# Kernel tuning notes

Hardware: AMD Instinct MI355X
Metric: run time of the kernel (lower is better)

The kernel has to match this reference:

```python
import jax, jax.numpy as jnp
import numpy as np

N_NODES = 100000


def setup_inputs() -> dict:
    key = jax.random.key(0)
    k_x, k_r, k_c, k_v, k_t = jax.random.split(key, 5)
    n_edges = 3200000
    fin, fout = 512, 128
    x = jax.random.normal(k_x, (N_NODES, fin), dtype=jnp.float32)
    rows = jax.random.randint(k_r, (n_edges,), 0, N_NODES, dtype=jnp.int32)
    cols = jax.random.randint(k_c, (n_edges,), 0, N_NODES, dtype=jnp.int32)
    vals = jax.random.uniform(k_v, (n_edges,), dtype=jnp.float32)
    theta = jax.random.normal(k_t, (fin, fout), dtype=jnp.float32) * (1.0 / np.sqrt(fin))
    bias = jnp.zeros((fout,), dtype=jnp.float32)
    return {"x": x, "rows": rows, "cols": cols, "vals": vals, "theta": theta, "bias": bias}


def reference(x, rows, cols, vals, theta, bias):
    # SpMM: mx[i] = sum over edges (i <- j) of A[i,j] * x[j]
    gathered = vals[:, None] * x[cols]                      # [E, fin]
    mx = jax.ops.segment_sum(gathered, rows, num_segments=N_NODES)  # [N, fin]
    # Dense feature transform + bias + relu
    o = jnp.einsum('nf,fo->no', mx, theta) + bias           # [N, fout]
    return jax.nn.relu(o)
```

## Files before the change

### kernel.cpp

```cpp
#include <hip/hip_runtime.h>
#include <stdint.h>
#include <stddef.h>

#define FIN 512
#define FOUT 128
#define BROWS 160
#define SORT_CAP 7680
#define TILE 4096
#define SCHUNK 1024

typedef __attribute__((ext_vector_type(8))) short short8;
typedef __attribute__((ext_vector_type(4))) float f32x4;

__device__ __forceinline__ unsigned short f2bf(float f) {
  unsigned u = __builtin_bit_cast(unsigned, f);
  u = (u + 0x7fffu + ((u >> 16) & 1u)) >> 16;
  return (unsigned short)u;
}
__device__ __forceinline__ float bf2f(unsigned short h) {
  unsigned u = ((unsigned)h) << 16;
  return __builtin_bit_cast(float, u);
}

__global__ void prep_theta_k(const float* __restrict__ theta,
                             unsigned short* __restrict__ thetaT) {
  int idx = blockIdx.x * blockDim.x + threadIdx.x;
  int n = idx >> 9;
  int k = idx & 511;
  thetaT[idx] = f2bf(theta[k * FOUT + n]);
}

__global__ __launch_bounds__(256) void gemm_k(const float* __restrict__ x,
                                              const unsigned short* __restrict__ thetaT,
                                              unsigned short* __restrict__ yb, int M) {
  __shared__ __align__(16) unsigned short lA[128 * 40];
  __shared__ __align__(16) unsigned short lB[128 * 40];
  const int tid = threadIdx.x;
  const int row0 = blockIdx.x * 128;
  const int wave = tid >> 6, lane = tid & 63;
  const int wm = wave >> 1, wn = wave & 1;
  const int fr = lane & 15, fq = lane >> 4;
  const int arow = tid >> 1, ahalf = tid & 1;

  f32x4 acc[4][4] = {};

  const int grow = row0 + arow;
  const bool aval = (grow < M);
  const float* asrc = x + (size_t)(aval ? grow : 0) * FIN + ahalf * 16;
  const unsigned short* bsrc = thetaT + (size_t)arow * FIN + ahalf * 16;

  for (int k0 = 0; k0 < FIN; k0 += 32) {
    float av[16];
    if (aval) {
      const float4* p = (const float4*)(asrc + k0);
      float4 v0 = p[0], v1 = p[1], v2 = p[2], v3 = p[3];
      av[0] = v0.x; av[1] = v0.y; av[2] = v0.z; av[3] = v0.w;
      av[4] = v1.x; av[5] = v1.y; av[6] = v1.z; av[7] = v1.w;
      av[8] = v2.x; av[9] = v2.y; av[10] = v2.z; av[11] = v2.w;
      av[12] = v3.x; av[13] = v3.y; av[14] = v3.z; av[15] = v3.w;
    } else {
      for (int i = 0; i < 16; i++) av[i] = 0.f;
    }
    unsigned ap[8];
    for (int i = 0; i < 8; i++)
      ap[i] = (unsigned)f2bf(av[2 * i]) | ((unsigned)f2bf(av[2 * i + 1]) << 16);
    uint4* aw = (uint4*)&lA[arow * 40 + ahalf * 16];
    aw[0] = make_uint4(ap[0], ap[1], ap[2], ap[3]);
    aw[1] = make_uint4(ap[4], ap[5], ap[6], ap[7]);

    const uint4* bp = (const uint4*)(bsrc + k0);
    uint4 b0 = bp[0], b1 = bp[1];
    uint4* bw = (uint4*)&lB[arow * 40 + ahalf * 16];
    bw[0] = b0; bw[1] = b1;

    __syncthreads();

    short8 af[4], bfv[4];
#pragma unroll
    for (int m = 0; m < 4; m++)
      af[m] = *(const short8*)&lA[(wm * 64 + m * 16 + fr) * 40 + fq * 8];
#pragma unroll
    for (int n = 0; n < 4; n++)
      bfv[n] = *(const short8*)&lB[(wn * 64 + n * 16 + fr) * 40 + fq * 8];
#pragma unroll
    for (int m = 0; m < 4; m++)
#pragma unroll
      for (int n = 0; n < 4; n++)
        acc[m][n] = __builtin_amdgcn_mfma_f32_16x16x32_bf16(af[m], bfv[n], acc[m][n], 0, 0, 0);

    __syncthreads();
  }

#pragma unroll
  for (int m = 0; m < 4; m++) {
    int rbase = row0 + wm * 64 + m * 16 + fq * 4;
#pragma unroll
    for (int j = 0; j < 4; j++) {
      int r = rbase + j;
      if (r < M) {
        unsigned short* dst = yb + (size_t)r * FOUT + wn * 64;
#pragma unroll
        for (int n = 0; n < 4; n++) dst[n * 16 + fr] = f2bf(acc[m][n][j]);
      }
    }
  }
}

__global__ __launch_bounds__(256) void chist_k(const int* __restrict__ rows,
                                               int* __restrict__ cnt,
                                               int E, int NT, int NB) {
  __shared__ int lh[1024];
  int c = blockIdx.x, t = threadIdx.x;
  for (int i = t; i < NB; i += 256) lh[i] = 0;
  __syncthreads();
  int base = c * TILE;
#pragma unroll
  for (int k = 0; k < TILE / 256; k++) {
    int i = base + k * 256 + t;
    if (i < E) atomicAdd(&lh[rows[i] / BROWS], 1);
  }
  __syncthreads();
  for (int j = t; j < NB; j += 256) cnt[(size_t)j * NT + c] = lh[j];
}

__global__ __launch_bounds__(256) void scan_partial_k(const int* __restrict__ counts,
                                                      int* __restrict__ blockSums, int N) {
  int base = blockIdx.x * SCHUNK;
  int t = threadIdx.x;
  int s = 0;
#pragma unroll
  for (int i = 0; i < SCHUNK / 256; i++) {
    int idx = base + t + i * 256;
    s += (idx < N) ? counts[idx] : 0;
  }
  for (int off = 32; off; off >>= 1) s += __shfl_down(s, off, 64);
  __shared__ int ws[4];
  if ((t & 63) == 0) ws[t >> 6] = s;
  __syncthreads();
  if (t == 0) blockSums[blockIdx.x] = ws[0] + ws[1] + ws[2] + ws[3];
}

__global__ __launch_bounds__(1024) void scan_sums_k(int* __restrict__ blockSums, int nb) {
  __shared__ int tmp[1024];
  int t = threadIdx.x;
  tmp[t] = (t < nb) ? blockSums[t] : 0;
  __syncthreads();
  for (int off = 1; off < 1024; off <<= 1) {
    int v = (t >= off) ? tmp[t - off] : 0;
    __syncthreads();
    tmp[t] += v;
    __syncthreads();
  }
  if (t < nb) blockSums[t] = (t == 0) ? 0 : tmp[t - 1];
}

__global__ __launch_bounds__(256) void scan_final_k(const int* __restrict__ counts,
                                                    const int* __restrict__ blockSums,
                                                    int* __restrict__ pos, int N) {
  int b = blockIdx.x;
  int t = threadIdx.x;
  int idx = b * SCHUNK + t * 4;
  int v0 = (idx + 0 < N) ? counts[idx + 0] : 0;
  int v1 = (idx + 1 < N) ? counts[idx + 1] : 0;
  int v2 = (idx + 2 < N) ? counts[idx + 2] : 0;
  int v3 = (idx + 3 < N) ? counts[idx + 3] : 0;
  int local = v0 + v1 + v2 + v3;

  int lane = t & 63, w = t >> 6;
  int inc = local;
  for (int off = 1; off < 64; off <<= 1) {
    int u = __shfl_up(inc, off, 64);
    if (lane >= off) inc += u;
  }
  __shared__ int wsum[4];
  if (lane == 63) wsum[w] = inc;
  __syncthreads();
  int woff = 0;
  for (int i = 0; i < 4; i++)
    if (i < w) woff += wsum[i];
  int run = blockSums[b] + woff + inc - local;

  if (idx + 0 < N) pos[idx + 0] = run; run += v0;
  if (idx + 1 < N) pos[idx + 1] = run; run += v1;
  if (idx + 2 < N) pos[idx + 2] = run; run += v2;
  if (idx + 3 < N) pos[idx + 3] = run; run += v3;
}

__global__ __launch_bounds__(256) void bmeta_k(const int* __restrict__ pos,
                                               int* __restrict__ boff,
                                               int* __restrict__ offsets,
                                               int NB, int NT, int E, int M) {
  int t = threadIdx.x;
  for (int b = t; b < NB; b += 256) boff[b] = pos[(size_t)b * NT];
  if (t == 0) {
    boff[NB] = E;
    offsets[M] = E;
  }
}

__global__ __launch_bounds__(256) void cscatter_k(const int* __restrict__ rows,
                                                  const int* __restrict__ cols,
                                                  const float* __restrict__ vals,
                                                  const int* __restrict__ pos,
                                                  unsigned* __restrict__ rec4,
                                                  unsigned char* __restrict__ rlo,
                                                  int E, int NT, int NB) {
  __shared__ int cur[1024];
  int c = blockIdx.x, t = threadIdx.x;
  for (int i = t; i < NB; i += 256) cur[i] = pos[(size_t)i * NT + c];
  __syncthreads();
  int base = c * TILE;
#pragma unroll
  for (int k = 0; k < TILE / 256; k++) {
    int i = base + k * 256 + t;
    if (i < E) {
      int r = rows[i];
      int b = r / BROWS;
      int p = atomicAdd(&cur[b], 1);
      rec4[p] = ((unsigned)cols[i] << 15) | ((unsigned)f2bf(vals[i]) & 0x7fffu);
      rlo[p] = (unsigned char)(r - b * BROWS);
    }
  }
}

__global__ __launch_bounds__(256) void bsort_k(const int* __restrict__ boff,
                                               unsigned* __restrict__ rec4,
                                               const unsigned char* __restrict__ rlo,
                                               int* __restrict__ offsets, int M) {
  __shared__ unsigned s4[SORT_CAP];
  __shared__ unsigned char k8[SORT_CAP];
  __shared__ int lh[256];
  __shared__ int lsc[256];
  int b = blockIdx.x, t = threadIdx.x;
  int start = boff[b], end = boff[b + 1];
  int n = end - start;
  if (n > SORT_CAP) n = SORT_CAP;

  for (int i = t; i < n; i += 256) {
    s4[i] = rec4[start + i];
    k8[i] = rlo[start + i];
  }
  lh[t] = 0;
  __syncthreads();
  for (int i = t; i < n; i += 256) atomicAdd(&lh[k8[i]], 1);
  __syncthreads();
  lsc[t] = lh[t];
  __syncthreads();
  for (int off = 1; off < 256; off <<= 1) {
    int v = (t >= off) ? lsc[t - off] : 0;
    __syncthreads();
    lsc[t] += v;
    __syncthreads();
  }
  int excl = t ? lsc[t - 1] : 0;
  int row = b * BROWS + t;
  if (t < BROWS && row < M) offsets[row] = start + excl;
  lh[t] = excl;
  __syncthreads();
  for (int i = t; i < n; i += 256) {
    unsigned r = s4[i];
    int p = atomicAdd(&lh[k8[i]], 1);
    rec4[start + p] = r;
  }
}

__global__ __launch_bounds__(256) void rowv2_k(const int* __restrict__ offsets,
                                               const unsigned* __restrict__ rec4,
                                               const unsigned short* __restrict__ yb,
                                               const float* __restrict__ bias,
                                               float* __restrict__ out, int M) {
  int gid = blockIdx.x * blockDim.x + threadIdx.x;
  int r = gid >> 4;
  int l = gid & 15;
  if (r >= M) return;
  int s = offsets[r], e = offsets[r + 1];
  const unsigned short* src = yb + l * 8;

  float a0 = 0.f, a1 = 0.f, a2 = 0.f, a3 = 0.f, a4 = 0.f, a5 = 0.f, a6 = 0.f, a7 = 0.f;
  float c0 = 0.f, c1 = 0.f, c2 = 0.f, c3 = 0.f, c4 = 0.f, c5 = 0.f, c6 = 0.f, c7 = 0.f;

  int i = s;
  for (; i + 2 <= e; i += 2) {
    unsigned q0 = rec4[i];
    unsigned q1 = rec4[i + 1];
    const uint4 u0 = *(const uint4*)(src + (size_t)(q0 >> 15) * FOUT);
    const uint4 u1 = *(const uint4*)(src + (size_t)(q1 >> 15) * FOUT);
    float v0 = __builtin_bit_cast(float, (q0 & 0x7fffu) << 16);
    float v1 = __builtin_bit_cast(float, (q1 & 0x7fffu) << 16);
    a0 += v0 * __builtin_bit_cast(float, u0.x << 16);
    a1 += v0 * __builtin_bit_cast(float, u0.x & 0xffff0000u);
    a2 += v0 * __builtin_bit_cast(float, u0.y << 16);
    a3 += v0 * __builtin_bit_cast(float, u0.y & 0xffff0000u);
    a4 += v0 * __builtin_bit_cast(float, u0.z << 16);
    a5 += v0 * __builtin_bit_cast(float, u0.z & 0xffff0000u);
    a6 += v0 * __builtin_bit_cast(float, u0.w << 16);
    a7 += v0 * __builtin_bit_cast(float, u0.w & 0xffff0000u);
    c0 += v1 * __builtin_bit_cast(float, u1.x << 16);
    c1 += v1 * __builtin_bit_cast(float, u1.x & 0xffff0000u);
    c2 += v1 * __builtin_bit_cast(float, u1.y << 16);
    c3 += v1 * __builtin_bit_cast(float, u1.y & 0xffff0000u);
    c4 += v1 * __builtin_bit_cast(float, u1.z << 16);
    c5 += v1 * __builtin_bit_cast(float, u1.z & 0xffff0000u);
    c6 += v1 * __builtin_bit_cast(float, u1.w << 16);
    c7 += v1 * __builtin_bit_cast(float, u1.w & 0xffff0000u);
  }
  if (i < e) {
    unsigned q0 = rec4[i];
    const uint4 u0 = *(const uint4*)(src + (size_t)(q0 >> 15) * FOUT);
    float v0 = __builtin_bit_cast(float, (q0 & 0x7fffu) << 16);
    a0 += v0 * __builtin_bit_cast(float, u0.x << 16);
    a1 += v0 * __builtin_bit_cast(float, u0.x & 0xffff0000u);
    a2 += v0 * __builtin_bit_cast(float, u0.y << 16);
    a3 += v0 * __builtin_bit_cast(float, u0.y & 0xffff0000u);
    a4 += v0 * __builtin_bit_cast(float, u0.z << 16);
    a5 += v0 * __builtin_bit_cast(float, u0.z & 0xffff0000u);
    a6 += v0 * __builtin_bit_cast(float, u0.w << 16);
    a7 += v0 * __builtin_bit_cast(float, u0.w & 0xffff0000u);
  }

  const float4 b0 = *(const float4*)(bias + l * 8);
  const float4 b1 = *(const float4*)(bias + l * 8 + 4);
  float* dst = out + (size_t)r * FOUT + l * 8;
  float4 o0, o1;
  o0.x = fmaxf(a0 + c0 + b0.x, 0.f);
  o0.y = fmaxf(a1 + c1 + b0.y, 0.f);
  o0.z = fmaxf(a2 + c2 + b0.z, 0.f);
  o0.w = fmaxf(a3 + c3 + b0.w, 0.f);
  o1.x = fmaxf(a4 + c4 + b1.x, 0.f);
  o1.y = fmaxf(a5 + c5 + b1.y, 0.f);
  o1.z = fmaxf(a6 + c6 + b1.z, 0.f);
  o1.w = fmaxf(a7 + c7 + b1.w, 0.f);
  *(float4*)(dst) = o0;
  *(float4*)(dst + 4) = o1;
}

extern "C" void kernel_launch(void* const* d_in, const int* in_sizes, int n_in,
                              void* d_out, int out_size, void* d_ws, size_t ws_size,
                              hipStream_t stream) {
  const float* x = (const float*)d_in[0];
  const int* rows = (const int*)d_in[1];
  const int* cols = (const int*)d_in[2];
  const float* vals = (const float*)d_in[3];
  const float* theta = (const float*)d_in[4];
  const float* bias = (const float*)d_in[5];
  float* out = (float*)d_out;
  const int M = in_sizes[0] / FIN;
  const int E = in_sizes[1];
  const int NB = (M + BROWS - 1) / BROWS;
  const int NT = (E + TILE - 1) / TILE;

  char* w = (char*)d_ws;
  auto alloc = [&](size_t bytes) {
    char* p = w;
    w += (bytes + 255) & ~(size_t)255;
    return p;
  };
  unsigned short* yb = (unsigned short*)alloc((size_t)M * FOUT * 2);
  unsigned short* thetaT = (unsigned short*)alloc((size_t)FIN * FOUT * 2);
  int* cnt = (int*)alloc((size_t)NB * NT * 4);
  int* pos = (int*)alloc((size_t)NB * NT * 4);
  int* boff = (int*)alloc((size_t)(NB + 1) * 4);
  int* offsets = (int*)alloc((size_t)(M + 1) * 4);
  unsigned* rec4 = (unsigned*)alloc((size_t)E * 4);
  unsigned char* rlo = (unsigned char*)alloc((size_t)E);
  const int NSCAN = NB * NT;
  const int nb2 = (NSCAN + SCHUNK - 1) / SCHUNK;
  int* blockSums = (int*)alloc((size_t)nb2 * 4);

  prep_theta_k<<<(FIN * FOUT) / 256, 256, 0, stream>>>(theta, thetaT);
  gemm_k<<<(M + 127) / 128, 256, 0, stream>>>(x, thetaT, yb, M);
  chist_k<<<NT, 256, 0, stream>>>(rows, cnt, E, NT, NB);
  scan_partial_k<<<nb2, 256, 0, stream>>>(cnt, blockSums, NSCAN);
  scan_sums_k<<<1, 1024, 0, stream>>>(blockSums, nb2);
  scan_final_k<<<nb2, 256, 0, stream>>>(cnt, blockSums, pos, NSCAN);
  bmeta_k<<<1, 256, 0, stream>>>(pos, boff, offsets, NB, NT, E, M);
  cscatter_k<<<NT, 256, 0, stream>>>(rows, cols, vals, pos, rec4, rlo, E, NT, NB);
  bsort_k<<<NB, 256, 0, stream>>>(boff, rec4, rlo, offsets, M);
  rowv2_k<<<(M * 16 + 255) / 256, 256, 0, stream>>>(offsets, rec4, yb, bias, out, M);
}
```

Baseline: 361.9 us.

## Coarsen bucket-count matrix to edge slices and scatter via global atomic cursors

Replaces the per-tile bucket count matrix (NB x NT) with a coarser NB x K matrix where K counts 128K-edge slices. Tile histograms are merged into it with global atomics, and the scatter claims slots through global atomic cursors instead of per-block shared-memory cursors. The aim is to shrink the prefix scan and the count/pos traffic. The cost is a memset, contended global atomics in the scatter, and a scatter order within a bucket that is no longer deterministic (bsort sorts it afterwards).

Result: slower. 412.3 us (+13.9%).

```diff
diff --git a/kernel.cpp b/kernel.cpp
--- a/kernel.cpp
+++ b/kernel.cpp
@@ -7,6 +7,7 @@
 #define BROWS 160
 #define SORT_CAP 7680
 #define TILE 4096
+#define SLICE_SHIFT 17
 #define SCHUNK 1024
 
 typedef __attribute__((ext_vector_type(8))) short short8;
@@ -107,20 +108,22 @@
 }
 
 __global__ __launch_bounds__(256) void chist_k(const int* __restrict__ rows,
-                                               int* __restrict__ cnt,
-                                               int E, int NT, int NB) {
+                                               int* __restrict__ cnt2,
+                                               int E, int K) {
   __shared__ int lh[1024];
   int c = blockIdx.x, t = threadIdx.x;
-  for (int i = t; i < NB; i += 256) lh[i] = 0;
+  int k = c >> 5;
+  for (int i = t; i < 1024; i += 256) lh[i] = 0;
   __syncthreads();
   int base = c * TILE;
 #pragma unroll
-  for (int k = 0; k < TILE / 256; k++) {
-    int i = base + k * 256 + t;
+  for (int kk = 0; kk < TILE / 256; kk++) {
+    int i = base + kk * 256 + t;
     if (i < E) atomicAdd(&lh[rows[i] / BROWS], 1);
   }
   __syncthreads();
-  for (int j = t; j < NB; j += 256) cnt[(size_t)j * NT + c] = lh[j];
+  for (int j = t; j < 1024; j += 256)
+    if (lh[j]) atomicAdd(&cnt2[(size_t)j * K + k], lh[j]);
 }
 
 __global__ __launch_bounds__(256) void scan_partial_k(const int* __restrict__ counts,
@@ -156,7 +159,8 @@
 
 __global__ __launch_bounds__(256) void scan_final_k(const int* __restrict__ counts,
                                                     const int* __restrict__ blockSums,
-                                                    int* __restrict__ pos, int N) {
+                                                    int* __restrict__ pos,
+                                                    int* __restrict__ gcur, int N) {
   int b = blockIdx.x;
   int t = threadIdx.x;
   int idx = b * SCHUNK + t * 4;
@@ -180,18 +184,18 @@
     if (i < w) woff += wsum[i];
   int run = blockSums[b] + woff + inc - local;
 
-  if (idx + 0 < N) pos[idx + 0] = run; run += v0;
-  if (idx + 1 < N) pos[idx + 1] = run; run += v1;
-  if (idx + 2 < N) pos[idx + 2] = run; run += v2;
-  if (idx + 3 < N) pos[idx + 3] = run; run += v3;
+  if (idx + 0 < N) { pos[idx + 0] = run; gcur[idx + 0] = run; } run += v0;
+  if (idx + 1 < N) { pos[idx + 1] = run; gcur[idx + 1] = run; } run += v1;
+  if (idx + 2 < N) { pos[idx + 2] = run; gcur[idx + 2] = run; } run += v2;
+  if (idx + 3 < N) { pos[idx + 3] = run; gcur[idx + 3] = run; } run += v3;
 }
 
 __global__ __launch_bounds__(256) void bmeta_k(const int* __restrict__ pos,
                                                int* __restrict__ boff,
                                                int* __restrict__ offsets,
-                                               int NB, int NT, int E, int M) {
+                                               int NB, int K, int E, int M) {
   int t = threadIdx.x;
-  for (int b = t; b < NB; b += 256) boff[b] = pos[(size_t)b * NT];
+  for (int b = t; b < NB; b += 256) boff[b] = pos[(size_t)b * K];
   if (t == 0) {
     boff[NB] = E;
     offsets[M] = E;
@@ -201,25 +205,19 @@
 __global__ __launch_bounds__(256) void cscatter_k(const int* __restrict__ rows,
                                                   const int* __restrict__ cols,
                                                   const float* __restrict__ vals,
-                                                  const int* __restrict__ pos,
+                                                  int* __restrict__ gcur,
                                                   unsigned* __restrict__ rec4,
                                                   unsigned char* __restrict__ rlo,
-                                                  int E, int NT, int NB) {
-  __shared__ int cur[1024];
-  int c = blockIdx.x, t = threadIdx.x;
-  for (int i = t; i < NB; i += 256) cur[i] = pos[(size_t)i * NT + c];
-  __syncthreads();
-  int base = c * TILE;
-#pragma unroll
-  for (int k = 0; k < TILE / 256; k++) {
-    int i = base + k * 256 + t;
-    if (i < E) {
-      int r = rows[i];
-      int b = r / BROWS;
-      int p = atomicAdd(&cur[b], 1);
-      rec4[p] = ((unsigned)cols[i] << 15) | ((unsigned)f2bf(vals[i]) & 0x7fffu);
-      rlo[p] = (unsigned char)(r - b * BROWS);
-    }
+                                                  int E, int K) {
+  int i = blockIdx.x * blockDim.x + threadIdx.x;
+  int st = gridDim.x * blockDim.x;
+  for (; i < E; i += st) {
+    int r = rows[i];
+    int b = r / BROWS;
+    int k = i >> SLICE_SHIFT;
+    int p = atomicAdd(&gcur[(size_t)b * K + k], 1);
+    rec4[p] = ((unsigned)cols[i] << 15) | ((unsigned)f2bf(vals[i]) & 0x7fffu);
+    rlo[p] = (unsigned char)(r - b * BROWS);
   }
 }
 
@@ -348,6 +346,7 @@
   const int E = in_sizes[1];
   const int NB = (M + BROWS - 1) / BROWS;
   const int NT = (E + TILE - 1) / TILE;
+  const int K = (E + (1 << SLICE_SHIFT) - 1) >> SLICE_SHIFT;
 
   char* w = (char*)d_ws;
   auto alloc = [&](size_t bytes) {
@@ -357,24 +356,26 @@
   };
   unsigned short* yb = (unsigned short*)alloc((size_t)M * FOUT * 2);
   unsigned short* thetaT = (unsigned short*)alloc((size_t)FIN * FOUT * 2);
-  int* cnt = (int*)alloc((size_t)NB * NT * 4);
-  int* pos = (int*)alloc((size_t)NB * NT * 4);
+  const int NSCAN = NB * K;
+  int* cnt2 = (int*)alloc((size_t)NSCAN * 4);
+  int* pos = (int*)alloc((size_t)NSCAN * 4);
+  int* gcur = (int*)alloc((size_t)NSCAN * 4);
   int* boff = (int*)alloc((size_t)(NB + 1) * 4);
   int* offsets = (int*)alloc((size_t)(M + 1) * 4);
   unsigned* rec4 = (unsigned*)alloc((size_t)E * 4);
   unsigned char* rlo = (unsigned char*)alloc((size_t)E);
-  const int NSCAN = NB * NT;
   const int nb2 = (NSCAN + SCHUNK - 1) / SCHUNK;
   int* blockSums = (int*)alloc((size_t)nb2 * 4);
 
+  hipMemsetAsync(cnt2, 0, (size_t)NSCAN * 4, stream);
   prep_theta_k<<<(FIN * FOUT) / 256, 256, 0, stream>>>(theta, thetaT);
   gemm_k<<<(M + 127) / 128, 256, 0, stream>>>(x, thetaT, yb, M);
-  chist_k<<<NT, 256, 0, stream>>>(rows, cnt, E, NT, NB);
-  scan_partial_k<<<nb2, 256, 0, stream>>>(cnt, blockSums, NSCAN);
+  chist_k<<<NT, 256, 0, stream>>>(rows, cnt2, E, K);
+  scan_partial_k<<<nb2, 256, 0, stream>>>(cnt2, blockSums, NSCAN);
   scan_sums_k<<<1, 1024, 0, stream>>>(blockSums, nb2);
-  scan_final_k<<<nb2, 256, 0, stream>>>(cnt, blockSums, pos, NSCAN);
-  bmeta_k<<<1, 256, 0, stream>>>(pos, boff, offsets, NB, NT, E, M);
-  cscatter_k<<<NT, 256, 0, stream>>>(rows, cols, vals, pos, rec4, rlo, E, NT, NB);
+  scan_final_k<<<nb2, 256, 0, stream>>>(cnt2, blockSums, pos, gcur, NSCAN);
+  bmeta_k<<<1, 256, 0, stream>>>(pos, boff, offsets, NB, K, E, M);
+  cscatter_k<<<2048, 256, 0, stream>>>(rows, cols, vals, gcur, rec4, rlo, E, K);
   bsort_k<<<NB, 256, 0, stream>>>(boff, rec4, rlo, offsets, M);
   rowv2_k<<<(M * 16 + 255) / 256, 256, 0, stream>>>(offsets, rec4, yb, bias, out, M);
 }
```

## Replace global bucket scan and scatter with per-tile LDS bucket sort plus merge

Applied to the files above, without the earlier changes.

Edges are now bucketed in a single tile-local pass. Each 8192-edge tile histograms, scans and scatters its records into shared memory, then writes them contiguously along with per-tile bucket offsets. One small kernel sums the per-bucket totals. The bucket-sort kernel then gathers each bucket's segments from all tiles before doing the row-level sort. This drops the multi-kernel global scan (histogram, three scan passes, meta, scatter) and the random global scatter. In exchange, bucket-sort threads run serial per-tile copy loops, the single-block totals kernel loops over all ~391 tiles, and NBK is hardcoded to 625 buckets.

After: 344.2 us. -4.9%, faster.

```diff
diff --git a/kernel.cpp b/kernel.cpp
--- a/kernel.cpp
+++ b/kernel.cpp
@@ -5,9 +5,9 @@
 #define FIN 512
 #define FOUT 128
 #define BROWS 160
+#define NBK 625
 #define SORT_CAP 7680
-#define TILE 4096
-#define SCHUNK 1024
+#define TILE 8192
 
 typedef __attribute__((ext_vector_type(8))) short short8;
 typedef __attribute__((ext_vector_type(4))) float f32x4;
@@ -106,142 +106,170 @@
   }
 }
 
-__global__ __launch_bounds__(256) void chist_k(const int* __restrict__ rows,
-                                               int* __restrict__ cnt,
-                                               int E, int NT, int NB) {
-  __shared__ int lh[1024];
-  int c = blockIdx.x, t = threadIdx.x;
-  for (int i = t; i < NB; i += 256) lh[i] = 0;
-  __syncthreads();
-  int base = c * TILE;
+__global__ __launch_bounds__(256) void tilesort_k(const int* __restrict__ rows,
+                                                  const int* __restrict__ cols,
+                                                  const float* __restrict__ vals,
+                                                  unsigned* __restrict__ rec4tile,
+                                                  unsigned char* __restrict__ rlotile,
+                                                  int* __restrict__ lofs, int E) {
+  __shared__ int hist[NBK];
+  __shared__ int wsum[4];
+  __shared__ unsigned srec[TILE];
+  __shared__ unsigned char srlo[TILE];
+  const int c = blockIdx.x, t = threadIdx.x;
+  const int base = c * TILE;
+  const int n = (E - base < TILE) ? (E - base) : TILE;
+
+  for (int i = t; i < NBK; i += 256) hist[i] = 0;
+  __syncthreads();
+
 #pragma unroll
   for (int k = 0; k < TILE / 256; k++) {
     int i = base + k * 256 + t;
-    if (i < E) atomicAdd(&lh[rows[i] / BROWS], 1);
-  }
-  __syncthreads();
-  for (int j = t; j < NB; j += 256) cnt[(size_t)j * NT + c] = lh[j];
-}
-
-__global__ __launch_bounds__(256) void scan_partial_k(const int* __restrict__ counts,
-                                                      int* __restrict__ blockSums, int N) {
-  int base = blockIdx.x * SCHUNK;
-  int t = threadIdx.x;
-  int s = 0;
-#pragma unroll
-  for (int i = 0; i < SCHUNK / 256; i++) {
-    int idx = base + t + i * 256;
-    s += (idx < N) ? counts[idx] : 0;
-  }
-  for (int off = 32; off; off >>= 1) s += __shfl_down(s, off, 64);
-  __shared__ int ws[4];
-  if ((t & 63) == 0) ws[t >> 6] = s;
-  __syncthreads();
-  if (t == 0) blockSums[blockIdx.x] = ws[0] + ws[1] + ws[2] + ws[3];
-}
-
-__global__ __launch_bounds__(1024) void scan_sums_k(int* __restrict__ blockSums, int nb) {
-  __shared__ int tmp[1024];
-  int t = threadIdx.x;
-  tmp[t] = (t < nb) ? blockSums[t] : 0;
-  __syncthreads();
-  for (int off = 1; off < 1024; off <<= 1) {
-    int v = (t >= off) ? tmp[t - off] : 0;
-    __syncthreads();
-    tmp[t] += v;
-    __syncthreads();
-  }
-  if (t < nb) blockSums[t] = (t == 0) ? 0 : tmp[t - 1];
-}
-
-__global__ __launch_bounds__(256) void scan_final_k(const int* __restrict__ counts,
-                                                    const int* __restrict__ blockSums,
-                                                    int* __restrict__ pos, int N) {
-  int b = blockIdx.x;
-  int t = threadIdx.x;
-  int idx = b * SCHUNK + t * 4;
-  int v0 = (idx + 0 < N) ? counts[idx + 0] : 0;
-  int v1 = (idx + 1 < N) ? counts[idx + 1] : 0;
-  int v2 = (idx + 2 < N) ? counts[idx + 2] : 0;
-  int v3 = (idx + 3 < N) ? counts[idx + 3] : 0;
-  int local = v0 + v1 + v2 + v3;
-
-  int lane = t & 63, w = t >> 6;
-  int inc = local;
+    if (i < E) atomicAdd(&hist[rows[i] / BROWS], 1);
+  }
+  __syncthreads();
+
+  int c0 = t * 3, c1 = c0 + 1, c2 = c0 + 2;
+  int h0 = (c0 < NBK) ? hist[c0] : 0;
+  int h1 = (c1 < NBK) ? hist[c1] : 0;
+  int h2 = (c2 < NBK) ? hist[c2] : 0;
+  int loc = h0 + h1 + h2;
+  int lane = t & 63, wv = t >> 6;
+  int inc = loc;
   for (int off = 1; off < 64; off <<= 1) {
     int u = __shfl_up(inc, off, 64);
     if (lane >= off) inc += u;
   }
-  __shared__ int wsum[4];
-  if (lane == 63) wsum[w] = inc;
-  __syncthreads();
-  int woff = 0;
+  if (lane == 63) wsum[wv] = inc;
+  __syncthreads();
+  int excl = inc - loc;
   for (int i = 0; i < 4; i++)
-    if (i < w) woff += wsum[i];
-  int run = blockSums[b] + woff + inc - local;
-
-  if (idx + 0 < N) pos[idx + 0] = run; run += v0;
-  if (idx + 1 < N) pos[idx + 1] = run; run += v1;
-  if (idx + 2 < N) pos[idx + 2] = run; run += v2;
-  if (idx + 3 < N) pos[idx + 3] = run; run += v3;
-}
-
-__global__ __launch_bounds__(256) void bmeta_k(const int* __restrict__ pos,
-                                               int* __restrict__ boff,
-                                               int* __restrict__ offsets,
-                                               int NB, int NT, int E, int M) {
-  int t = threadIdx.x;
-  for (int b = t; b < NB; b += 256) boff[b] = pos[(size_t)b * NT];
-  if (t == 0) {
-    boff[NB] = E;
-    offsets[M] = E;
-  }
-}
-
-__global__ __launch_bounds__(256) void cscatter_k(const int* __restrict__ rows,
-                                                  const int* __restrict__ cols,
-                                                  const float* __restrict__ vals,
-                                                  const int* __restrict__ pos,
-                                                  unsigned* __restrict__ rec4,
-                                                  unsigned char* __restrict__ rlo,
-                                                  int E, int NT, int NB) {
-  __shared__ int cur[1024];
-  int c = blockIdx.x, t = threadIdx.x;
-  for (int i = t; i < NB; i += 256) cur[i] = pos[(size_t)i * NT + c];
-  __syncthreads();
-  int base = c * TILE;
+    if (i < wv) excl += wsum[i];
+
+  size_t lbase = (size_t)c * (NBK + 1);
+  int e = excl;
+  if (c0 <= NBK) lofs[lbase + c0] = e;
+  __syncthreads();
+  if (c0 < NBK) hist[c0] = e;
+  e += h0;
+  if (c1 <= NBK) lofs[lbase + c1] = e;
+  if (c1 < NBK) hist[c1] = e;
+  e += h1;
+  if (c2 <= NBK) lofs[lbase + c2] = e;
+  if (c2 < NBK) hist[c2] = e;
+  __syncthreads();
+
 #pragma unroll
   for (int k = 0; k < TILE / 256; k++) {
     int i = base + k * 256 + t;
     if (i < E) {
       int r = rows[i];
       int b = r / BROWS;
-      int p = atomicAdd(&cur[b], 1);
-      rec4[p] = ((unsigned)cols[i] << 15) | ((unsigned)f2bf(vals[i]) & 0x7fffu);
-      rlo[p] = (unsigned char)(r - b * BROWS);
-    }
+      int p = atomicAdd(&hist[b], 1);
+      srec[p] = ((unsigned)cols[i] << 15) | ((unsigned)f2bf(vals[i]) & 0x7fffu);
+      srlo[p] = (unsigned char)(r - b * BROWS);
+    }
+  }
+  __syncthreads();
+
+  for (int j = t; j < n; j += 256) {
+    rec4tile[base + j] = srec[j];
+    rlotile[base + j] = srlo[j];
+  }
+}
+
+__global__ __launch_bounds__(1024) void btot_k(const int* __restrict__ lofs,
+                                               int* __restrict__ boff,
+                                               int* __restrict__ offsets,
+                                               int NT, int E, int M) {
+  __shared__ int tmp[1024];
+  int t = threadIdx.x;
+  int s = 0;
+  if (t < NBK) {
+    for (int c = 0; c < NT; c++) {
+      size_t lb = (size_t)c * (NBK + 1) + t;
+      s += lofs[lb + 1] - lofs[lb];
+    }
+  }
+  tmp[t] = s;
+  __syncthreads();
+  for (int off = 1; off < 1024; off <<= 1) {
+    int v = (t >= off) ? tmp[t - off] : 0;
+    __syncthreads();
+    tmp[t] += v;
+    __syncthreads();
+  }
+  if (t < NBK) boff[t] = (t == 0) ? 0 : tmp[t - 1];
+  if (t == 0) {
+    boff[NBK] = E;
+    offsets[M] = E;
   }
 }
 
 __global__ __launch_bounds__(256) void bsort_k(const int* __restrict__ boff,
-                                               unsigned* __restrict__ rec4,
-                                               const unsigned char* __restrict__ rlo,
-                                               int* __restrict__ offsets, int M) {
+                                               const int* __restrict__ lofs,
+                                               const unsigned* __restrict__ rec4tile,
+                                               const unsigned char* __restrict__ rlotile,
+                                               unsigned* __restrict__ rec4s,
+                                               int* __restrict__ offsets,
+                                               int NT, int M) {
   __shared__ unsigned s4[SORT_CAP];
   __shared__ unsigned char k8[SORT_CAP];
   __shared__ int lh[256];
   __shared__ int lsc[256];
+  __shared__ int wsum[4];
   int b = blockIdx.x, t = threadIdx.x;
-  int start = boff[b], end = boff[b + 1];
-  int n = end - start;
+  int start = boff[b];
+
+  int ca = 2 * t, cb = 2 * t + 1;
+  int la = 0, fa = 0, lb2 = 0, fb = 0;
+  if (ca < NT) {
+    size_t p = (size_t)ca * (NBK + 1) + b;
+    la = lofs[p];
+    fa = lofs[p + 1] - la;
+  }
+  if (cb < NT) {
+    size_t p = (size_t)cb * (NBK + 1) + b;
+    lb2 = lofs[p];
+    fb = lofs[p + 1] - lb2;
+  }
+  int loc = fa + fb;
+  int lane = t & 63, wv = t >> 6;
+  int inc = loc;
+  for (int off = 1; off < 64; off <<= 1) {
+    int u = __shfl_up(inc, off, 64);
+    if (lane >= off) inc += u;
+  }
+  if (lane == 63) wsum[wv] = inc;
+  __syncthreads();
+  int excl = inc - loc;
+  for (int i = 0; i < 4; i++)
+    if (i < wv) excl += wsum[i];
+
+  if (ca < NT) {
+    const unsigned* src = rec4tile + (size_t)ca * TILE + la;
+    const unsigned char* srl = rlotile + (size_t)ca * TILE + la;
+    for (int j = 0; j < fa; j++) {
+      int d = excl + j;
+      if (d < SORT_CAP) { s4[d] = src[j]; k8[d] = srl[j]; }
+    }
+    excl += fa;
+  }
+  if (cb < NT) {
+    const unsigned* src = rec4tile + (size_t)cb * TILE + lb2;
+    const unsigned char* srl = rlotile + (size_t)cb * TILE + lb2;
+    for (int j = 0; j < fb; j++) {
+      int d = excl + j;
+      if (d < SORT_CAP) { s4[d] = src[j]; k8[d] = srl[j]; }
+    }
+  }
+
+  int n = boff[b + 1] - start;
   if (n > SORT_CAP) n = SORT_CAP;
-
-  for (int i = t; i < n; i += 256) {
-    s4[i] = rec4[start + i];
-    k8[i] = rlo[start + i];
-  }
   lh[t] = 0;
   __syncthreads();
+
   for (int i = t; i < n; i += 256) atomicAdd(&lh[k8[i]], 1);
   __syncthreads();
   lsc[t] = lh[t];
@@ -252,15 +280,15 @@
     lsc[t] += v;
     __syncthreads();
   }
-  int excl = t ? lsc[t - 1] : 0;
+  int ex = t ? lsc[t - 1] : 0;
   int row = b * BROWS + t;
-  if (t < BROWS && row < M) offsets[row] = start + excl;
-  lh[t] = excl;
+  if (t < BROWS && row < M) offsets[row] = start + ex;
+  lh[t] = ex;
   __syncthreads();
   for (int i = t; i < n; i += 256) {
     unsigned r = s4[i];
     int p = atomicAdd(&lh[k8[i]], 1);
-    rec4[start + p] = r;
+    rec4s[start + p] = r;
   }
 }
 
@@ -346,7 +374,6 @@
   float* out = (float*)d_out;
   const int M = in_sizes[0] / FIN;
   const int E = in_sizes[1];
-  const int NB = (M + BROWS - 1) / BROWS;
   const int NT = (E + TILE - 1) / TILE;
 
   char* w = (char*)d_ws;
@@ -357,24 +384,17 @@
   };
   unsigned short* yb = (unsigned short*)alloc((size_t)M * FOUT * 2);
   unsigned short* thetaT = (unsigned short*)alloc((size_t)FIN * FOUT * 2);
-  int* cnt = (int*)alloc((size_t)NB * NT * 4);
-  int* pos = (int*)alloc((size_t)NB * NT * 4);
-  int* boff = (int*)alloc((size_t)(NB + 1) * 4);
+  unsigned* rec4tile = (unsigned*)alloc((size_t)NT * TILE * 4);
+  unsigned char* rlotile = (unsigned char*)alloc((size_t)NT * TILE);
+  int* lofs = (int*)alloc((size_t)NT * (NBK + 1) * 4);
+  int* boff = (int*)alloc((size_t)(NBK + 1) * 4);
   int* offsets = (int*)alloc((size_t)(M + 1) * 4);
-  unsigned* rec4 = (unsigned*)alloc((size_t)E * 4);
-  unsigned char* rlo = (unsigned char*)alloc((size_t)E);
-  const int NSCAN = NB * NT;
-  const int nb2 = (NSCAN + SCHUNK - 1) / SCHUNK;
-  int* blockSums = (int*)alloc((size_t)nb2 * 4);
+  unsigned* rec4s = (unsigned*)alloc((size_t)E * 4);
 
   prep_theta_k<<<(FIN * FOUT) / 256, 256, 0, stream>>>(theta, thetaT);
   gemm_k<<<(M + 127) / 128, 256, 0, stream>>>(x, thetaT, yb, M);
-  chist_k<<<NT, 256, 0, stream>>>(rows, cnt, E, NT, NB);
-  scan_partial_k<<<nb2, 256, 0, stream>>>(cnt, blockSums, NSCAN);
-  scan_sums_k<<<1, 1024, 0, stream>>>(blockSums, nb2);
-  scan_final_k<<<nb2, 256, 0, stream>>>(cnt, blockSums, pos, NSCAN);
-  bmeta_k<<<1, 256, 0, stream>>>(pos, boff, offsets, NB, NT, E, M);
-  cscatter_k<<<NT, 256, 0, stream>>>(rows, cols, vals, pos, rec4, rlo, E, NT, NB);
-  bsort_k<<<NB, 256, 0, stream>>>(boff, rec4, rlo, offsets, M);
-  rowv2_k<<<(M * 16 + 255) / 256, 256, 0, stream>>>(offsets, rec4, yb, bias, out, M);
-}
+  tilesort_k<<<NT, 256, 0, stream>>>(rows, cols, vals, rec4tile, rlotile, lofs, E);
+  btot_k<<<1, 1024, 0, stream>>>(lofs, boff, offsets, NT, E, M);
+  bsort_k<<<NBK, 256, 0, stream>>>(boff, lofs, rec4tile, rlotile, rec4s, offsets, NT, M);
+  rowv2_k<<<(M * 16 + 255) / 256, 256, 0, stream>>>(offsets, rec4s, yb, bias, out, M);
+}
```
